# Kernel tuning notes

Hardware: AMD Instinct MI355X
Metric: run time of the kernel (lower is better)

Reference implementation:

```python
import jax, jax.numpy as jnp
import numpy as np

N_MEL = 80; ARNN = 1024; ADIM = 128; EMB = 512; PRE = 256; DRNN = 1024; NF = 32; KS = 31
B = 32; NCTX = 512; T = 500
PAD = (KS - 1) // 2


def setup_inputs() -> dict:
    key = jax.random.key(0)
    ks = jax.random.split(key, 20)
    g = lambda k, shape: jax.random.normal(k, shape, dtype=jnp.float32) * 0.02
    return {
        "memory": jax.random.normal(ks[0], (B, NCTX, EMB), dtype=jnp.float32),
        "decoder_inputs": jax.random.normal(ks[1], (B, N_MEL, T), dtype=jnp.float32),
        "mask": jnp.zeros((B, NCTX), dtype=bool),
        "prenet_w1": g(ks[2], (PRE, N_MEL)),
        "prenet_w2": g(ks[3], (PRE, PRE)),
        "arnn_wih": g(ks[4], (4 * ARNN, PRE + EMB)),
        "arnn_whh": g(ks[5], (4 * ARNN, ARNN)),
        "arnn_bih": jnp.zeros((4 * ARNN,), jnp.float32),
        "arnn_bhh": jnp.zeros((4 * ARNN,), jnp.float32),
        "q_w": g(ks[6], (ADIM, ARNN)),
        "m_w": g(ks[7], (ADIM, EMB)),
        "loc_conv_w": g(ks[8], (NF, 2, KS)),
        "loc_w": g(ks[9], (ADIM, NF)),
        "v_w": g(ks[10], (ADIM,)),
        "drnn_wih": g(ks[11], (4 * DRNN, ARNN + EMB)),
        "drnn_whh": g(ks[12], (4 * DRNN, DRNN)),
        "drnn_bih": jnp.zeros((4 * DRNN,), jnp.float32),
        "drnn_bhh": jnp.zeros((4 * DRNN,), jnp.float32),
        "proj_w": g(ks[13], (N_MEL, DRNN + EMB)),
        "proj_b": jnp.zeros((N_MEL,), jnp.float32),
        "gate_w": g(ks[14], (1, DRNN + EMB)),
        "gate_b": jnp.zeros((1,), jnp.float32),
    }


def _lstm_cell(x, h, c, wih, whh, bih, bhh):
    # PyTorch LSTMCell gate order: i, f, g, o
    z = x @ wih.T + h @ whh.T + bih + bhh
    i, f, g, o = jnp.split(z, 4, axis=-1)
    c2 = jax.nn.sigmoid(f) * c + jax.nn.sigmoid(i) * jnp.tanh(g)
    h2 = jax.nn.sigmoid(o) * jnp.tanh(c2)
    return h2, c2


def reference(memory, decoder_inputs, mask,
              prenet_w1, prenet_w2,
              arnn_wih, arnn_whh, arnn_bih, arnn_bhh,
              q_w, m_w, loc_conv_w, loc_w, v_w,
              drnn_wih, drnn_whh, drnn_bih, drnn_bhh,
              proj_w, proj_b, gate_w, gate_b):
    b, n_ctx, emb = memory.shape
    n_mel, t_out = decoder_inputs.shape[1], decoder_inputs.shape[2]

    # (time, batch, n_mel) with a leading zero go-frame; PreNet (eval: no dropout)
    x = jnp.transpose(decoder_inputs, (2, 0, 1))
    x = jnp.concatenate([jnp.zeros((1, b, n_mel), x.dtype), x], axis=0)
    h = jax.nn.relu(x @ prenet_w1.T)
    h = jax.nn.relu(h @ prenet_w2.T)  # (T+1, B, PRE)
    inputs = h[:-1]  # T decoder steps

    proc_mem = memory @ m_w.T  # (B, n_ctx, ADIM)

    def step(carry, xin):
        ah, ac, dh, dc, aw, awc, actx = carry
        cell_in = jnp.concatenate([xin, actx], axis=-1)
        ah, ac = _lstm_cell(cell_in, ah, ac, arnn_wih, arnn_whh, arnn_bih, arnn_bhh)
        # location-sensitive attention
        aw_cat = jnp.stack([aw, awc], axis=1)  # (B, 2, n_ctx)
        loc = jax.lax.conv_general_dilated(
            aw_cat, loc_conv_w, window_strides=(1,), padding=[(PAD, PAD)],
            dimension_numbers=("NCH", "OIH", "NCH"))  # (B, NF, n_ctx)
        loc = jnp.transpose(loc, (0, 2, 1)) @ loc_w.T  # (B, n_ctx, ADIM)
        q = (ah @ q_w.T)[:, None, :]  # (B, 1, ADIM)
        e = jnp.tanh(q + proc_mem + loc) @ v_w  # (B, n_ctx)
        e = jnp.where(mask, -1e9, e)
        aw = jax.nn.softmax(e, axis=-1)
        actx = jnp.einsum("bn,bne->be", aw, memory)
        awc = awc + aw
        din = jnp.concatenate([ah, actx], axis=-1)
        dh, dc = _lstm_cell(din, dh, dc, drnn_wih, drnn_whh, drnn_bih, drnn_bhh)
        dhc = jnp.concatenate([dh, actx], axis=-1)
        mel = dhc @ proj_w.T + proj_b  # (B, n_mel)
        gate = dhc @ gate_w.T + gate_b  # (B, 1)
        return (ah, ac, dh, dc, aw, awc, actx), (mel, gate[:, 0])

    z32 = lambda *s: jnp.zeros(s, memory.dtype)
    carry0 = (z32(b, ARNN), z32(b, ARNN), z32(b, DRNN), z32(b, DRNN),
              z32(b, n_ctx), z32(b, n_ctx), z32(b, emb))
    _, (mels, gates) = jax.lax.scan(step, carry0, inputs)
    mel_out = jnp.transpose(mels, (1, 2, 0))   # (B, n_mel, T)
    gate_out = jnp.transpose(gates, (1, 0))    # (B, T)
    return mel_out, gate_out
```

## Files before the change

### kernel.cpp

```cpp
#include <hip/hip_runtime.h>

#define NBLK 256
#define NTHR 1024

constexpr int kNMel = 80, kArnn = 1024, kAdim = 128, kEmb = 512, kPre = 256;
constexpr int kNF = 32, kKS = 31, kB = 32, kNctx = 512, kT = 500, kPad = 15;

constexpr int KT_A = 56;
constexpr int KT_D = 80;
constexpr int KT_ALL = KT_A + KT_D;

constexpr int OFF_PREB   = 0;
constexpr int OFF_PROCMB = OFF_PREB + kT * kB * kPre / 2;
constexpr int OFF_QWTB   = OFF_PROCMB + kB * kNctx * kAdim / 2;
constexpr int OFF_LWT    = OFF_QWTB + kAdim * kArnn / 2;
constexpr int OFF_STATE  = OFF_LWT + kAdim * 33;
constexpr int OFF_AHB    = OFF_STATE;
constexpr int OFF_DHB    = OFF_AHB + 2 * kB * kArnn / 2;
constexpr int OFF_DH     = OFF_DHB + 2 * kB * kArnn / 2;
constexpr int OFF_AC     = OFF_DH + 2 * kB * kArnn;
constexpr int OFF_DC     = OFF_AC + kB * kArnn;
constexpr int OFF_ACTX   = OFF_DC + kB * kArnn;
constexpr int OFF_AW     = OFF_ACTX + kB * kEmb;
constexpr int OFF_AWC    = OFF_AW + kB * kNctx;
constexpr int OFF_PAW    = OFF_AWC + kB * kNctx;
constexpr int OFF_NUM    = OFF_PAW + kB * kNctx;
constexpr int OFF_DEN    = OFF_NUM + 2 * kB * kEmb;
constexpr int OFF_END    = OFF_DEN + 2 * kB;
constexpr int STATE_SZ   = OFF_END - OFF_STATE;
constexpr int OFF_BAR    = OFF_END;
constexpr int BAR_LINES  = 266;
constexpr int OFF_PAN    = OFF_BAR + BAR_LINES * 32;
constexpr int PAN_SZ     = NBLK * KT_ALL * 256;
constexpr int OFF_GMB    = OFF_PAN + PAN_SZ;
constexpr int GMB_SZ     = kB * kNctx * kEmb / 2;

typedef __attribute__((ext_vector_type(4))) float fvec4;
typedef __attribute__((ext_vector_type(8))) short bh8_t;
typedef unsigned long long u64;
typedef unsigned short ushortt;

union U64u { u64 u; float2 f2; ushortt s[4]; };

union SMem {
  struct { ushortt xs[16][2048]; } x1;
  struct { float zra[8][2][64][4]; float zrd[8][2][64][4];
           float hb[2][32][4]; } x2;
  struct { float ahb_s[kArnn]; float vw_s[kAdim]; float psum[1024]; float q_s[kAdim];
           float aw_s[96]; float awc_s[96]; float cw[kNF * 2 * kKS];
           float loc_s[64 * 33]; float p_s[64]; float lwt[kAdim * 33];
           float dhc[kArnn + kEmb]; float pprj[126];
           ushortt pm[64 * kAdim]; } b;
  struct { float x8[8][80]; float h1[8][256]; } p;
  struct { float mem_s[4][512]; } m;
};

__device__ __forceinline__ float sigf(float x) { return 1.0f / (1.0f + __expf(-x)); }
__device__ __forceinline__ float tanhfast(float x) { return 1.0f - 2.0f / (__expf(2.0f * x) + 1.0f); }

__device__ __forceinline__ ushortt bf16rn(float f) {
  unsigned u = __float_as_uint(f);
  unsigned r = (u + 0x7FFFu + ((u >> 16) & 1u)) >> 16;
  return (ushortt)r;
}
__device__ __forceinline__ float bf2f(ushortt v) {
  return __uint_as_float((unsigned)v << 16);
}

__device__ __forceinline__ u64 ald64(const void* p) {
  return __hip_atomic_load((const u64*)p, __ATOMIC_RELAXED, __HIP_MEMORY_SCOPE_AGENT);
}
__device__ __forceinline__ float alf(const float* p) {
  return __hip_atomic_load(p, __ATOMIC_RELAXED, __HIP_MEMORY_SCOPE_AGENT);
}
__device__ __forceinline__ void asf(float* p, float v) {
  __hip_atomic_store(p, v, __ATOMIC_RELAXED, __HIP_MEMORY_SCOPE_AGENT);
}
__device__ __forceinline__ void as64(void* p, u64 v) {
  __hip_atomic_store((u64*)p, v, __ATOMIC_RELAXED, __HIP_MEMORY_SCOPE_AGENT);
}
__device__ __forceinline__ unsigned alu(const unsigned* p) {
  return __hip_atomic_load(p, __ATOMIC_RELAXED, __HIP_MEMORY_SCOPE_AGENT);
}
__device__ __forceinline__ void asu(unsigned* p, unsigned v) {
  __hip_atomic_store(p, v, __ATOMIC_RELAXED, __HIP_MEMORY_SCOPE_AGENT);
}

__device__ __forceinline__ void gbar_full(unsigned* cnt, unsigned* gen, unsigned& genv) {
  __syncthreads();
  if (threadIdx.x == 0) {
    __threadfence();
    unsigned arrived = __hip_atomic_fetch_add(cnt, 1u, __ATOMIC_ACQ_REL, __HIP_MEMORY_SCOPE_AGENT) + 1u;
    if (arrived == (unsigned)NBLK) {
      __hip_atomic_store(cnt, 0u, __ATOMIC_RELAXED, __HIP_MEMORY_SCOPE_AGENT);
      __hip_atomic_fetch_add(gen, 1u, __ATOMIC_ACQ_REL, __HIP_MEMORY_SCOPE_AGENT);
    } else {
      while (__hip_atomic_load(gen, __ATOMIC_ACQUIRE, __HIP_MEMORY_SCOPE_AGENT) == genv) {
        __builtin_amdgcn_s_sleep(2);
      }
    }
    ++genv;
  }
  __syncthreads();
}

__device__ __forceinline__ void gbar_light(unsigned* bar, unsigned target, int bk, int tid) {
  asm volatile("s_waitcnt vmcnt(0) lgkmcnt(0)" ::: "memory");
  __syncthreads();
  if (bk == 0) {
    if (tid < 64) {
      if (tid == 0) asm volatile("s_waitcnt vmcnt(0)" ::: "memory");
      unsigned i0 = (unsigned)tid * 4, i1 = i0 + 1, i2 = i0 + 2, i3 = i0 + 3;
      for (;;) {
        bool ok = true;
        if (i0 != 0) ok = ok && (alu(&bar[i0 * 32]) >= target);
        ok = ok && (alu(&bar[i1 * 32]) >= target);
        ok = ok && (alu(&bar[i2 * 32]) >= target);
        ok = ok && (alu(&bar[i3 * 32]) >= target);
        if (__all(ok)) break;
        __builtin_amdgcn_s_sleep(1);
      }
      if (tid < 8) asu(&bar[(256 + tid) * 32], target);
    }
  } else {
    if (tid == 0) {
      asm volatile("s_waitcnt vmcnt(0)" ::: "memory");
      asu(&bar[bk * 32], target);
      unsigned* wk = &bar[(256 + (bk & 7)) * 32];
      while (alu(wk) < target) __builtin_amdgcn_s_sleep(1);
    }
  }
  __syncthreads();
}

template<int LS, int W>
__device__ __forceinline__ void lstm_wave(
    const ushortt* __restrict__ s0, const ushortt* __restrict__ s2,
    const float* __restrict__ numq, const float* __restrict__ invden,
    const short* __restrict__ pan,
    int l, ushortt* xs, fvec4& z0, fvec4& z1)
{
  constexpr int NC  = LS ? 5 : (W < 4 ? 4 : 3);
  constexpr int CB  = LS ? W * 320 : (W < 4 ? W * 256 : 1024 + (W - 4) * 192);
  constexpr int KT0 = CB / 32;
  constexpr int BD0 = LS ? 1024 : 256;
  constexpr int BD1 = LS ? 1536 : 768;
  const int u8 = l & 15, rj = l >> 4;
  const int m = l & 15, kg = l >> 4;

  #pragma unroll
  for (int c = 0; c < NC; ++c) {
    const int c0 = CB + c * 64;
    u64 L[8];
    if (c0 >= BD0 && c0 < BD1) {
      const float* base = numq + (c0 - BD0) + u8 * 4;
      #pragma unroll
      for (int j = 0; j < 8; ++j) {
        int row = 4 * j + rj;
        const float* fp = base + (size_t)row * kEmb;
        U64u a, b2; a.u = ald64(fp); b2.u = ald64(fp + 2);
        float s = invden[row];
        U64u pk;
        pk.s[0] = bf16rn(a.f2.x * s);  pk.s[1] = bf16rn(a.f2.y * s);
        pk.s[2] = bf16rn(b2.f2.x * s); pk.s[3] = bf16rn(b2.f2.y * s);
        L[j] = pk.u;
      }
    } else {
      const ushortt* bsrc; int stride; bool coh;
      if (c0 < BD0) { bsrc = s0 + c0;       stride = (LS ? 1024 : 256); coh = (LS == 1); }
      else          { bsrc = s2 + c0 - BD1; stride = 1024;              coh = true; }
      #pragma unroll
      for (int j = 0; j < 8; ++j) {
        const ushortt* ap = bsrc + (size_t)(4 * j + rj) * stride + u8 * 4;
        L[j] = coh ? ald64(ap) : *reinterpret_cast<const u64*>(ap);
      }
    }
    bh8_t f0 = *reinterpret_cast<const bh8_t*>(pan + (size_t)(KT0 + c * 2) * 512 + l * 8);
    bh8_t f1 = *reinterpret_cast<const bh8_t*>(pan + (size_t)(KT0 + c * 2 + 1) * 512 + l * 8);
    #pragma unroll
    for (int j = 0; j < 8; ++j) {
      int row = 4 * j + rj;
      int sw = u8 ^ ((row & 7) << 1);
      *reinterpret_cast<u64*>(xs + row * 64 + sw * 4) = L[j];
    }
    #pragma unroll
    for (int kt = 0; kt < 2; ++kt) {
      int sw = (2 * (kt * 4 + kg)) ^ ((m & 7) << 1);
      bh8_t a0 = *reinterpret_cast<const bh8_t*>(xs + m * 64 + sw * 4);
      bh8_t a1 = *reinterpret_cast<const bh8_t*>(xs + (16 + m) * 64 + sw * 4);
      bh8_t f = kt ? f1 : f0;
      z0 = __builtin_amdgcn_mfma_f32_16x16x32_bf16(a0, f, z0, 0, 0, 0);
      z1 = __builtin_amdgcn_mfma_f32_16x16x32_bf16(a1, f, z1, 0, 0, 0);
    }
  }
}

extern "C" __global__ void __launch_bounds__(NTHR, 4)
decoder_kernel(const float* __restrict__ gmem, const float* __restrict__ dec,
               const unsigned char* __restrict__ mask,
               const float* __restrict__ pw1, const float* __restrict__ pw2,
               const float* __restrict__ awih, const float* __restrict__ awhh,
               const float* __restrict__ abih, const float* __restrict__ abhh,
               const float* __restrict__ qw, const float* __restrict__ mw,
               const float* __restrict__ cvw, const float* __restrict__ locw,
               const float* __restrict__ vw,
               const float* __restrict__ dwih, const float* __restrict__ dwhh,
               const float* __restrict__ dbih, const float* __restrict__ dbhh,
               const float* __restrict__ pjw, const float* __restrict__ pjb,
               const float* __restrict__ gw, const float* __restrict__ gb,
               float* __restrict__ out, float* __restrict__ ws, int useg)
{
  __shared__ SMem sm;
  __shared__ float s_invden[32];
  const int bk = blockIdx.x, tid = threadIdx.x;
  unsigned genv_f = 0, bcnt = 0;
  unsigned* bar = reinterpret_cast<unsigned*>(ws + OFF_BAR);
  unsigned* cntF = &bar[264 * 32];
  unsigned* genF = &bar[265 * 32];

  ushortt* PREBu = reinterpret_cast<ushortt*>(ws + OFF_PREB);
  ushortt* PROCMBu = reinterpret_cast<ushortt*>(ws + OFF_PROCMB);
  ushortt* QWTBu = reinterpret_cast<ushortt*>(ws + OFF_QWTB);
  float* LWT = ws + OFF_LWT;
  ushortt* AHBu = reinterpret_cast<ushortt*>(ws + OFF_AHB);
  ushortt* DHBu = reinterpret_cast<ushortt*>(ws + OFF_DHB);
  float* DH = ws + OFF_DH;
  float* AC = ws + OFF_AC;
  float* DC = ws + OFF_DC;
  float* ACTX = ws + OFF_ACTX;
  float* AWp = ws + OFF_AW;
  float* AWC = ws + OFF_AWC;
  float* PAW = ws + OFF_PAW;
  float* NUM = ws + OFF_NUM;
  float* DEN = ws + OFF_DEN;
  short* PANS = reinterpret_cast<short*>(ws + OFF_PAN);
  ushortt* GMB = reinterpret_cast<ushortt*>(ws + OFF_GMB);

  for (int i = bk * NTHR + tid; i < STATE_SZ; i += NBLK * NTHR) (ws + OFF_STATE)[i] = 0.f;
  for (int i = bk * NTHR + tid; i < kAdim * kArnn; i += NBLK * NTHR)
    QWTBu[i] = bf16rn(qw[i]);
  for (int i = bk * NTHR + tid; i < kAdim * kNF; i += NBLK * NTHR) {
    int d = i >> 5, f = i & 31;
    LWT[d * 33 + f] = locw[i];
  }
  gbar_full(cntF, genF, genv_f);

  if (bk == 0 && tid < 2 * kB) asf(&DEN[tid], 1.0f);
  for (int it = 0; it < 16; ++it) {
    int task0 = bk * 64 + it * 4;
    for (int i = tid; i < 2048; i += NTHR) {
      int pr = i >> 9, h = i & 511;
      sm.m.mem_s[pr][h] = gmem[(size_t)(task0 + pr) * kEmb + h];
    }
    __syncthreads();
    if (tid < 512) {
      int pr = tid >> 7, d = tid & 127;
      const float* mwr = mw + d * kEmb;
      float acc = 0.f;
      for (int h = 0; h < kEmb; ++h) acc = fmaf(sm.m.mem_s[pr][h], mwr[h], acc);
      PROCMBu[(size_t)(task0 + pr) * kAdim + d] = bf16rn(acc);
    }
    if (useg) {
      for (int i = tid; i < 2048; i += NTHR) {
        int pr = i >> 9, h = i & 511;
        GMB[(size_t)(task0 + pr) * kEmb + h] = bf16rn(sm.m.mem_s[pr][h]);
      }
    }
    __syncthreads();
  }
  for (int g = bk; g < 2000; g += NBLK) {
    int t_idx = g >> 2;
    int b0 = (g & 3) * 8;
    if (t_idx == 0) {
      for (int i = tid; i < 8 * kPre; i += NTHR)
        PREBu[(size_t)(b0 + (i >> 8)) * kPre + (i & 255)] = 0;
      continue;
    }
    for (int i = tid; i < 640; i += NTHR) {
      int bb = i / 80, m2 = i % 80;
      sm.p.x8[bb][m2] = dec[((size_t)(b0 + bb) * kNMel + m2) * kT + (t_idx - 1)];
    }
    __syncthreads();
    if (tid < 512) {
      int u = tid & 255, rep = tid >> 8;
      float acc[4] = {0.f, 0.f, 0.f, 0.f};
      for (int m2 = 0; m2 < 80; ++m2) {
        float w = pw1[u * kNMel + m2];
        #pragma unroll
        for (int r = 0; r < 4; ++r) acc[r] = fmaf(w, sm.p.x8[rep * 4 + r][m2], acc[r]);
      }
      #pragma unroll
      for (int r = 0; r < 4; ++r) sm.p.h1[rep * 4 + r][u] = fmaxf(acc[r], 0.f);
    }
    __syncthreads();
    if (tid < 512) {
      int u = tid & 255, rep = tid >> 8;
      float acc[4] = {0.f, 0.f, 0.f, 0.f};
      for (int k = 0; k < kPre; ++k) {
        float w = pw2[u * kPre + k];
        #pragma unroll
        for (int r = 0; r < 4; ++r) acc[r] = fmaf(w, sm.p.h1[rep * 4 + r][k], acc[r]);
      }
      #pragma unroll
      for (int r = 0; r < 4; ++r)
        PREBu[((size_t)t_idx * kB + b0 + rep * 4 + r) * kPre + u] = bf16rn(fmaxf(acc[r], 0.f));
    }
    __syncthreads();
  }
  {
    const int UNITS = NBLK * KT_ALL * 64;
    for (int u = bk * NTHR + tid; u < UNITS; u += NBLK * NTHR) {
      int bkk = u / (KT_ALL * 64);
      int rem = u - bkk * (KT_ALL * 64);
      int kta = rem >> 6, l = rem & 63;
      int lstm = (kta >= KT_A);
      int kt = lstm ? kta - KT_A : kta;
      int n = l & 15, kg = l >> 4;
      int r = (n >> 2) * 1024 + bkk * 4 + (n & 3);
      bh8_t v;
      #pragma unroll
      for (int j = 0; j < 8; ++j) {
        int k = kt * 32 + kg * 8 + j;
        float wv;
        if (!lstm) wv = (k < 768) ? awih[(size_t)r * 768 + k] : awhh[(size_t)r * 1024 + (k - 768)];
        else       wv = (k < 1536) ? dwih[(size_t)r * 1536 + k] : dwhh[(size_t)r * 1024 + (k - 1536)];
        v[j] = (short)bf16rn(wv);
      }
      *reinterpret_cast<bh8_t*>(PANS + (size_t)u * 8) = v;
    }
  }
  gbar_full(cntF, genF, genv_f);

  for (int t = 0; t <= kT; ++t) {
    const int p = t & 1, q = p ^ 1;
    float* nump = NUM + p * kB * kEmb;
    const float* numq = NUM + q * kB * kEmb;

    if (tid < kB) s_invden[tid] = 1.0f / alf(DEN + q * kB + tid);
    __syncthreads();
    if (t > 0 && tid < 64) {
      int idx = bk * 64 + tid;
      int b2 = idx >> 9;
      float invd = s_invden[b2];
      float av = PAW[idx] * invd;
      asf(&AWp[idx], av);
      asf(&AWC[idx], alf(&AWC[idx]) + av);
      asf(&ACTX[idx], alf(&numq[idx]) * invd);
    }
    if (t < kT) {
      if (tid < 64) asf(&nump[bk * 64 + tid], 0.f);
      if (bk == 0 && tid < kB) asf(DEN + p * kB + tid, 0.f);
    }
    {
      const int wid = tid >> 6, l = tid & 63;
      fvec4 z0 = {0.f, 0.f, 0.f, 0.f}, z1 = z0;
      const ushortt* AHBq_ = AHBu + q * kB * kArnn;
      const ushortt* DHBp_ = DHBu + p * kB * kArnn;
      const ushortt* preb_t = PREBu + (size_t)t * kB * kPre;
      ushortt* xs = &sm.x1.xs[wid][0];
      const short* panb = PANS + (size_t)bk * (KT_ALL * 512);
      const short* pand = panb + KT_A * 512;
      if (wid < 8) {
        if (t < kT) {
          switch (wid) {
            case 0: lstm_wave<0,0>(preb_t, AHBq_, numq, s_invden, panb, l, xs, z0, z1); break;
            case 1: lstm_wave<0,1>(preb_t, AHBq_, numq, s_invden, panb, l, xs, z0, z1); break;
            case 2: lstm_wave<0,2>(preb_t, AHBq_, numq, s_invden, panb, l, xs, z0, z1); break;
            case 3: lstm_wave<0,3>(preb_t, AHBq_, numq, s_invden, panb, l, xs, z0, z1); break;
            case 4: lstm_wave<0,4>(preb_t, AHBq_, numq, s_invden, panb, l, xs, z0, z1); break;
            case 5: lstm_wave<0,5>(preb_t, AHBq_, numq, s_invden, panb, l, xs, z0, z1); break;
            case 6: lstm_wave<0,6>(preb_t, AHBq_, numq, s_invden, panb, l, xs, z0, z1); break;
            default: lstm_wave<0,7>(preb_t, AHBq_, numq, s_invden, panb, l, xs, z0, z1); break;
          }
        }
      } else {
        if (t > 0) {
          switch (wid) {
            case 8:  lstm_wave<1,0>(AHBq_, DHBp_, numq, s_invden, pand, l, xs, z0, z1); break;
            case 9:  lstm_wave<1,1>(AHBq_, DHBp_, numq, s_invden, pand, l, xs, z0, z1); break;
            case 10: lstm_wave<1,2>(AHBq_, DHBp_, numq, s_invden, pand, l, xs, z0, z1); break;
            case 11: lstm_wave<1,3>(AHBq_, DHBp_, numq, s_invden, pand, l, xs, z0, z1); break;
            case 12: lstm_wave<1,4>(AHBq_, DHBp_, numq, s_invden, pand, l, xs, z0, z1); break;
            case 13: lstm_wave<1,5>(AHBq_, DHBp_, numq, s_invden, pand, l, xs, z0, z1); break;
            case 14: lstm_wave<1,6>(AHBq_, DHBp_, numq, s_invden, pand, l, xs, z0, z1); break;
            default: lstm_wave<1,7>(AHBq_, DHBp_, numq, s_invden, pand, l, xs, z0, z1); break;
          }
        }
      }
      __syncthreads();
      if (wid < 8) {
        *reinterpret_cast<fvec4*>(&sm.x2.zra[wid][0][l][0]) = z0;
        *reinterpret_cast<fvec4*>(&sm.x2.zra[wid][1][l][0]) = z1;
      } else {
        *reinterpret_cast<fvec4*>(&sm.x2.zrd[wid - 8][0][l][0]) = z0;
        *reinterpret_cast<fvec4*>(&sm.x2.zrd[wid - 8][1][l][0]) = z1;
      }
    }
    __syncthreads();
    if (tid < 256) {
      const int ls = tid >> 7, uu = (tid >> 5) & 3, b = tid & 31;
      const bool go = (ls == 0) ? (t < kT) : (t > 0);
      if (go) {
        const int mt = b >> 4, mm = b & 15;
        const int lane_base = (mm >> 2) * 16, rr = mm & 3;
        float zg[4];
        #pragma unroll
        for (int g = 0; g < 4; ++g) {
          int ln = lane_base + g * 4 + uu;
          float s = 0.f;
          if (ls == 0) {
            #pragma unroll
            for (int w = 0; w < 8; ++w) s += sm.x2.zra[w][mt][ln][rr];
          } else {
            #pragma unroll
            for (int w = 0; w < 8; ++w) s += sm.x2.zrd[w][mt][ln][rr];
          }
          int rg = g * 1024 + bk * 4 + uu;
          s += (ls ? dbih[rg] + dbhh[rg] : abih[rg] + abhh[rg]);
          zg[g] = s;
        }
        float* cst = ls ? DC : AC;
        const int idx = b * kArnn + bk * 4 + uu;
        float c = sigf(zg[1]) * cst[idx] + sigf(zg[0]) * tanhfast(zg[2]);
        cst[idx] = c;
        float h = sigf(zg[3]) * tanhfast(c);
        if (ls) asf(&DH[q * kB * kArnn + idx], h);
        sm.x2.hb[ls][b][uu] = h;
      }
    }
    __syncthreads();
    if (tid < 64) {
      int ls = tid >> 5, b = tid & 31;
      bool go2 = ls ? (t > 0) : (t < kT);
      if (go2) {
        U64u pk;
        #pragma unroll
        for (int j = 0; j < 4; ++j) pk.s[j] = bf16rn(sm.x2.hb[ls][b][j]);
        ushortt* dst = (ls ? (DHBu + q * kB * kArnn) : (AHBu + p * kB * kArnn)) + b * kArnn + bk * 4;
        as64(dst, pk.u);
      }
    }
    gbar_light(bar, ++bcnt, bk, tid);

    if (t < kT) {
      const int b = bk >> 3, sub = bk & 7, j0 = sub * 64;
      const int pbase = (sub == 0) ? 0 : 21 + (sub - 1) * 20;
      const int pcnt = (sub == 0) ? 21 : 20;
      const ushortt* AHBp_ = AHBu + p * kB * kArnn;
      if (tid < 256) {
        U64u v; v.u = ald64(AHBp_ + b * kArnn + tid * 4);
        #pragma unroll
        for (int j = 0; j < 4; ++j) sm.b.ahb_s[tid * 4 + j] = bf2f(v.s[j]);
      }
      for (int i = tid; i < 94; i += NTHR) {
        int jj = j0 - kPad + i;
        bool ok = (jj >= 0 && jj < kNctx);
        sm.b.aw_s[i] = ok ? alf(&AWp[b * kNctx + jj]) : 0.f;
        sm.b.awc_s[i] = ok ? alf(&AWC[b * kNctx + jj]) : 0.f;
      }
      for (int i = tid; i < kNF * 2 * kKS; i += NTHR) sm.b.cw[i] = cvw[i];
      for (int i = tid; i < kAdim * 33; i += NTHR) sm.b.lwt[i] = LWT[i];
      for (int i = tid; i < kAdim; i += NTHR) sm.b.vw_s[i] = vw[i];
      {
        const fvec4* src = reinterpret_cast<const fvec4*>(PROCMBu + (size_t)(b * kNctx + j0) * kAdim);
        fvec4* dst = reinterpret_cast<fvec4*>(sm.b.pm);
        for (int i = tid; i < 1024; i += NTHR) dst[i] = src[i];
      }
      if (sub < 4 && t > 0) {
        for (int i = tid; i < kArnn + kEmb; i += NTHR)
          sm.b.dhc[i] = (i < kArnn) ? alf(&DH[q * kB * kArnn + b * kArnn + i])
                                    : alf(&ACTX[b * kEmb + (i - kArnn)]);
      }
      __syncthreads();
      {
        int d = tid & 127, qr = tid >> 7;
        const ushortt* wq = QWTBu + (size_t)d * kArnn + qr * 128;
        const float* ahs = sm.b.ahb_s + qr * 128;
        float acc = 0.f;
        #pragma unroll 4
        for (int h8 = 0; h8 < 16; ++h8) {
          U64u a, c2;
          a.u = *reinterpret_cast<const u64*>(wq + h8 * 8);
          c2.u = *reinterpret_cast<const u64*>(wq + h8 * 8 + 4);
          #pragma unroll
          for (int j = 0; j < 4; ++j) acc = fmaf(bf2f(a.s[j]), ahs[h8 * 8 + j], acc);
          #pragma unroll
          for (int j = 0; j < 4; ++j) acc = fmaf(bf2f(c2.s[j]), ahs[h8 * 8 + 4 + j], acc);
        }
        sm.b.psum[tid] = acc;
      }
      __syncthreads();
      if (tid < kAdim) {
        float s = 0.f;
        #pragma unroll
        for (int k = 0; k < 8; ++k) s += sm.b.psum[tid + 128 * k];
        sm.b.q_s[tid] = s;
      }
      if (tid < 512) {
        int j = tid >> 3, f0 = (tid & 7) * 4;
        #pragma unroll
        for (int fi = 0; fi < 4; ++fi) {
          int f = f0 + fi;
          const float* w0 = &sm.b.cw[f * 62];
          float s = 0.f;
          for (int k = 0; k < kKS; ++k)
            s = fmaf(sm.b.aw_s[j + k], w0[k], fmaf(sm.b.awc_s[j + k], w0[31 + k], s));
          sm.b.loc_s[j * 33 + f] = s;
        }
      }
      if (sub < 4 && t > 0 && tid < pcnt * 6) {
        int ol = tid / 6, kc = tid % 6, og = pbase + ol;
        const float* row = (og < kNMel) ? pjw + (size_t)og * (kArnn + kEmb) : gw;
        const float* x = sm.b.dhc + kc * 256;
        const float* r2 = row + kc * 256;
        float acc = 0.f;
        for (int k = 0; k < 256; ++k) acc = fmaf(r2[k], x[k], acc);
        sm.b.pprj[tid] = acc;
      }
      __syncthreads();
      if (tid < 512) {
        int j = tid >> 3, grp = tid & 7, jj = j0 + j;
        float pe = 0.f;
        #pragma unroll 4
        for (int dd = 0; dd < 16; ++dd) {
          int d = grp + 8 * dd;
          float l2 = 0.f;
          const float* ls2 = &sm.b.loc_s[j * 33];
          const float* lw2 = &sm.b.lwt[d * 33];
          #pragma unroll 8
          for (int f = 0; f < kNF; ++f) l2 = fmaf(ls2[f], lw2[f], l2);
          float x = sm.b.q_s[d] + bf2f(sm.b.pm[j * kAdim + d]) + l2;
          pe = fmaf(sm.b.vw_s[d], tanhfast(x), pe);
        }
        pe += __shfl_xor(pe, 1);
        pe += __shfl_xor(pe, 2);
        pe += __shfl_xor(pe, 4);
        if (grp == 0) {
          float pv = mask[b * kNctx + jj] ? 0.f : __expf(pe);
          sm.b.p_s[j] = pv;
          PAW[b * kNctx + jj] = pv;
        }
      }
      if (sub < 4 && t > 0 && tid < pcnt) {
        int og = pbase + tid;
        float val = (og < kNMel) ? pjb[og] : gb[0];
        #pragma unroll
        for (int kc = 0; kc < 6; ++kc) val += sm.b.pprj[tid * 6 + kc];
        if (og < kNMel) out[((size_t)b * kNMel + og) * kT + (t - 1)] = val;
        else out[(size_t)kB * kNMel * kT + b * kT + (t - 1)] = val;
      }
      __syncthreads();
      if (tid < 64) {
        float v = sm.b.p_s[tid];
        #pragma unroll
        for (int o = 1; o < 64; o <<= 1) v += __shfl_xor(v, o);
        if (tid == 0) atomicAdd(DEN + p * kB + b, v);
      }
      {
        int col = tid & 511, half = tid >> 9;
        int jbase = half * 32;
        if (useg) {
          const ushortt* memb = GMB + (size_t)(b * kNctx + j0 + jbase) * kEmb + col;
          float a0 = 0.f, a1 = 0.f, a2 = 0.f, a3 = 0.f;
          #pragma unroll 4
          for (int jj2 = 0; jj2 < 32; jj2 += 4) {
            a0 = fmaf(sm.b.p_s[jbase + jj2],     bf2f(memb[(size_t)jj2 * kEmb]), a0);
            a1 = fmaf(sm.b.p_s[jbase + jj2 + 1], bf2f(memb[(size_t)(jj2 + 1) * kEmb]), a1);
            a2 = fmaf(sm.b.p_s[jbase + jj2 + 2], bf2f(memb[(size_t)(jj2 + 2) * kEmb]), a2);
            a3 = fmaf(sm.b.p_s[jbase + jj2 + 3], bf2f(memb[(size_t)(jj2 + 3) * kEmb]), a3);
          }
          atomicAdd(&nump[b * kEmb + col], (a0 + a1) + (a2 + a3));
        } else {
          const float* memb = gmem + (size_t)(b * kNctx + j0 + jbase) * kEmb + col;
          float a0 = 0.f, a1 = 0.f;
          #pragma unroll 8
          for (int jj2 = 0; jj2 < 32; jj2 += 2) {
            a0 = fmaf(sm.b.p_s[jbase + jj2], memb[(size_t)jj2 * kEmb], a0);
            a1 = fmaf(sm.b.p_s[jbase + jj2 + 1], memb[(size_t)(jj2 + 1) * kEmb], a1);
          }
          atomicAdd(&nump[b * kEmb + col], a0 + a1);
        }
      }
      gbar_light(bar, ++bcnt, bk, tid);
    }
  }

  if (bk < kB) {
    const int b = bk;
    for (int i = tid; i < kArnn + kEmb; i += NTHR)
      sm.b.dhc[i] = (i < kArnn) ? alf(&DH[1 * kB * kArnn + b * kArnn + i])
                                : alf(&ACTX[b * kEmb + (i - kArnn)]);
    __syncthreads();
    if (tid < 486) {
      int ol = tid / 6, kc = tid % 6;
      const float* row = (ol < kNMel) ? pjw + (size_t)ol * (kArnn + kEmb) : gw;
      const float* x = sm.b.dhc + kc * 256;
      const float* r2 = row + kc * 256;
      float acc = 0.f;
      for (int k = 0; k < 256; ++k) acc = fmaf(r2[k], x[k], acc);
      sm.b.psum[tid] = acc;
    }
    __syncthreads();
    if (tid < 81) {
      float val = (tid < kNMel) ? pjb[tid] : gb[0];
      #pragma unroll
      for (int kc = 0; kc < 6; ++kc) val += sm.b.psum[tid * 6 + kc];
      if (tid < kNMel) out[((size_t)b * kNMel + tid) * kT + (kT - 1)] = val;
      else out[(size_t)kB * kNMel * kT + b * kT + (kT - 1)] = val;
    }
  }
}

extern "C" void kernel_launch(void* const* d_in, const int* in_sizes, int n_in,
                              void* d_out, int out_size, void* d_ws, size_t ws_size,
                              hipStream_t stream) {
  const float* gmem = (const float*)d_in[0];
  const float* dec = (const float*)d_in[1];
  const unsigned char* mask = (const unsigned char*)d_in[2];
  const float* pw1 = (const float*)d_in[3];
  const float* pw2 = (const float*)d_in[4];
  const float* awih = (const float*)d_in[5];
  const float* awhh = (const float*)d_in[6];
  const float* abih = (const float*)d_in[7];
  const float* abhh = (const float*)d_in[8];
  const float* qw = (const float*)d_in[9];
  const float* mw = (const float*)d_in[10];
  const float* cvw = (const float*)d_in[11];
  const float* locw = (const float*)d_in[12];
  const float* vw = (const float*)d_in[13];
  const float* dwih = (const float*)d_in[14];
  const float* dwhh = (const float*)d_in[15];
  const float* dbih = (const float*)d_in[16];
  const float* dbhh = (const float*)d_in[17];
  const float* pjw = (const float*)d_in[18];
  const float* pjb = (const float*)d_in[19];
  const float* gw = (const float*)d_in[20];
  const float* gb = (const float*)d_in[21];
  float* out = (float*)d_out;
  float* ws = (float*)d_ws;

  int useg = (ws_size >= (size_t)(OFF_GMB + GMB_SZ) * sizeof(float)) ? 1 : 0;

  hipMemsetAsync((char*)d_ws + (size_t)OFF_BAR * sizeof(float), 0,
                 (size_t)BAR_LINES * 128, stream);
  hipLaunchKernelGGL(decoder_kernel, dim3(NBLK), dim3(NTHR), 0, stream,
                     gmem, dec, mask, pw1, pw2, awih, awhh, abih, abhh, qw, mw,
                     cvw, locw, vw, dwih, dwhh, dbih, dbhh, pjw, pjb, gw, gb,
                     out, ws, useg);
}
```

Baseline: 43.28 ms.

## Keep each block's memory slice and processed-memory tile resident in LDS

Each persistent block now keeps its fixed 64-row slice of the encoder memory (as bf16) and of the processed memory in a dedicated LDS region, loaded once before the time loop. The per-step context-vector accumulation and attention-energy computation read from LDS instead of global or L2 memory. The two half-block partial sums are also combined in LDS before a single atomic add per column, halving the atomics. The trade-off is a large increase in static shared memory, about 80 KB more, which may reduce occupancy or exceed LDS limits alongside the existing unions. It also removes the fp32 fallback path that was used when the workspace was too small.

```diff
diff --git a/kernel.cpp b/kernel.cpp
--- a/kernel.cpp
+++ b/kernel.cpp
@@ -32,8 +32,6 @@
 constexpr int BAR_LINES  = 266;
 constexpr int OFF_PAN    = OFF_BAR + BAR_LINES * 32;
 constexpr int PAN_SZ     = NBLK * KT_ALL * 256;
-constexpr int OFF_GMB    = OFF_PAN + PAN_SZ;
-constexpr int GMB_SZ     = kB * kNctx * kEmb / 2;
 
 typedef __attribute__((ext_vector_type(4))) float fvec4;
 typedef __attribute__((ext_vector_type(8))) short bh8_t;
@@ -42,17 +40,20 @@
 
 union U64u { u64 u; float2 f2; ushortt s[4]; };
 
-union SMem {
-  struct { ushortt xs[16][2048]; } x1;
-  struct { float zra[8][2][64][4]; float zrd[8][2][64][4];
-           float hb[2][32][4]; } x2;
-  struct { float ahb_s[kArnn]; float vw_s[kAdim]; float psum[1024]; float q_s[kAdim];
-           float aw_s[96]; float awc_s[96]; float cw[kNF * 2 * kKS];
-           float loc_s[64 * 33]; float p_s[64]; float lwt[kAdim * 33];
-           float dhc[kArnn + kEmb]; float pprj[126];
-           ushortt pm[64 * kAdim]; } b;
-  struct { float x8[8][80]; float h1[8][256]; } p;
-  struct { float mem_s[4][512]; } m;
+struct SMemS {
+  ushortt gmb[64 * kEmb];
+  ushortt pm[64 * kAdim];
+  union {
+    struct { ushortt xs[16][2048]; } x1;
+    struct { float zra[8][2][64][4]; float zrd[8][2][64][4];
+             float hb[2][32][4]; } x2;
+    struct { float ahb_s[kArnn]; float vw_s[kAdim]; float psum[1024]; float q_s[kAdim];
+             float aw_s[96]; float awc_s[96]; float cw[kNF * 2 * kKS];
+             float loc_s[64 * 33]; float p_s[64]; float lwt[kAdim * 33];
+             float dhc[kArnn + kEmb]; float pprj[126]; } b;
+    struct { float x8[8][80]; float h1[8][256]; } p;
+    struct { float mem_s[4][512]; } m;
+  } u;
 };
 
 __device__ __forceinline__ float sigf(float x) { return 1.0f / (1.0f + __expf(-x)); }
@@ -208,9 +209,9 @@
                const float* __restrict__ dbih, const float* __restrict__ dbhh,
                const float* __restrict__ pjw, const float* __restrict__ pjb,
                const float* __restrict__ gw, const float* __restrict__ gb,
-               float* __restrict__ out, float* __restrict__ ws, int useg)
+               float* __restrict__ out, float* __restrict__ ws)
 {
-  __shared__ SMem sm;
+  __shared__ SMemS sm;
   __shared__ float s_invden[32];
   const int bk = blockIdx.x, tid = threadIdx.x;
   unsigned genv_f = 0, bcnt = 0;
@@ -234,7 +235,6 @@
   float* NUM = ws + OFF_NUM;
   float* DEN = ws + OFF_DEN;
   short* PANS = reinterpret_cast<short*>(ws + OFF_PAN);
-  ushortt* GMB = reinterpret_cast<ushortt*>(ws + OFF_GMB);
 
   for (int i = bk * NTHR + tid; i < STATE_SZ; i += NBLK * NTHR) (ws + OFF_STATE)[i] = 0.f;
   for (int i = bk * NTHR + tid; i < kAdim * kArnn; i += NBLK * NTHR)
@@ -250,24 +250,25 @@
     int task0 = bk * 64 + it * 4;
     for (int i = tid; i < 2048; i += NTHR) {
       int pr = i >> 9, h = i & 511;
-      sm.m.mem_s[pr][h] = gmem[(size_t)(task0 + pr) * kEmb + h];
+      sm.u.m.mem_s[pr][h] = gmem[(size_t)(task0 + pr) * kEmb + h];
     }
     __syncthreads();
     if (tid < 512) {
       int pr = tid >> 7, d = tid & 127;
       const float* mwr = mw + d * kEmb;
       float acc = 0.f;
-      for (int h = 0; h < kEmb; ++h) acc = fmaf(sm.m.mem_s[pr][h], mwr[h], acc);
+      for (int h = 0; h < kEmb; ++h) acc = fmaf(sm.u.m.mem_s[pr][h], mwr[h], acc);
       PROCMBu[(size_t)(task0 + pr) * kAdim + d] = bf16rn(acc);
     }
-    if (useg) {
-      for (int i = tid; i < 2048; i += NTHR) {
-        int pr = i >> 9, h = i & 511;
-        GMB[(size_t)(task0 + pr) * kEmb + h] = bf16rn(sm.m.mem_s[pr][h]);
-      }
-    }
-    __syncthreads();
-  }
+    __syncthreads();
+  }
+  for (int i = tid; i < 64 * kEmb; i += NTHR) {
+    int j = i >> 9, h = i & 511;
+    sm.gmb[i] = bf16rn(gmem[((size_t)bk * 64 + j) * kEmb + h]);
+  }
+  for (int i = tid; i < 64 * kAdim; i += NTHR)
+    sm.pm[i] = PROCMBu[(size_t)bk * 64 * kAdim + i];
+  __syncthreads();
   for (int g = bk; g < 2000; g += NBLK) {
     int t_idx = g >> 2;
     int b0 = (g & 3) * 8;
@@ -278,7 +279,7 @@
     }
     for (int i = tid; i < 640; i += NTHR) {
       int bb = i / 80, m2 = i % 80;
-      sm.p.x8[bb][m2] = dec[((size_t)(b0 + bb) * kNMel + m2) * kT + (t_idx - 1)];
+      sm.u.p.x8[bb][m2] = dec[((size_t)(b0 + bb) * kNMel + m2) * kT + (t_idx - 1)];
     }
     __syncthreads();
     if (tid < 512) {
@@ -287,10 +288,10 @@
       for (int m2 = 0; m2 < 80; ++m2) {
         float w = pw1[u * kNMel + m2];
         #pragma unroll
-        for (int r = 0; r < 4; ++r) acc[r] = fmaf(w, sm.p.x8[rep * 4 + r][m2], acc[r]);
+        for (int r = 0; r < 4; ++r) acc[r] = fmaf(w, sm.u.p.x8[rep * 4 + r][m2], acc[r]);
       }
       #pragma unroll
-      for (int r = 0; r < 4; ++r) sm.p.h1[rep * 4 + r][u] = fmaxf(acc[r], 0.f);
+      for (int r = 0; r < 4; ++r) sm.u.p.h1[rep * 4 + r][u] = fmaxf(acc[r], 0.f);
     }
     __syncthreads();
     if (tid < 512) {
@@ -299,7 +300,7 @@
       for (int k = 0; k < kPre; ++k) {
         float w = pw2[u * kPre + k];
         #pragma unroll
-        for (int r = 0; r < 4; ++r) acc[r] = fmaf(w, sm.p.h1[rep * 4 + r][k], acc[r]);
+        for (int r = 0; r < 4; ++r) acc[r] = fmaf(w, sm.u.p.h1[rep * 4 + r][k], acc[r]);
       }
       #pragma unroll
       for (int r = 0; r < 4; ++r)
@@ -357,7 +358,7 @@
       const ushortt* AHBq_ = AHBu + q * kB * kArnn;
       const ushortt* DHBp_ = DHBu + p * kB * kArnn;
       const ushortt* preb_t = PREBu + (size_t)t * kB * kPre;
-      ushortt* xs = &sm.x1.xs[wid][0];
+      ushortt* xs = &sm.u.x1.xs[wid][0];
       const short* panb = PANS + (size_t)bk * (KT_ALL * 512);
       const short* pand = panb + KT_A * 512;
       if (wid < 8) {
@@ -389,11 +390,11 @@
       }
       __syncthreads();
       if (wid < 8) {
-        *reinterpret_cast<fvec4*>(&sm.x2.zra[wid][0][l][0]) = z0;
-        *reinterpret_cast<fvec4*>(&sm.x2.zra[wid][1][l][0]) = z1;
+        *reinterpret_cast<fvec4*>(&sm.u.x2.zra[wid][0][l][0]) = z0;
+        *reinterpret_cast<fvec4*>(&sm.u.x2.zra[wid][1][l][0]) = z1;
       } else {
-        *reinterpret_cast<fvec4*>(&sm.x2.zrd[wid - 8][0][l][0]) = z0;
-        *reinterpret_cast<fvec4*>(&sm.x2.zrd[wid - 8][1][l][0]) = z1;
+        *reinterpret_cast<fvec4*>(&sm.u.x2.zrd[wid - 8][0][l][0]) = z0;
+        *reinterpret_cast<fvec4*>(&sm.u.x2.zrd[wid - 8][1][l][0]) = z1;
       }
     }
     __syncthreads();
@@ -410,10 +411,10 @@
           float s = 0.f;
           if (ls == 0) {
             #pragma unroll
-            for (int w = 0; w < 8; ++w) s += sm.x2.zra[w][mt][ln][rr];
+            for (int w = 0; w < 8; ++w) s += sm.u.x2.zra[w][mt][ln][rr];
           } else {
             #pragma unroll
-            for (int w = 0; w < 8; ++w) s += sm.x2.zrd[w][mt][ln][rr];
+            for (int w = 0; w < 8; ++w) s += sm.u.x2.zrd[w][mt][ln][rr];
           }
           int rg = g * 1024 + bk * 4 + uu;
           s += (ls ? dbih[rg] + dbhh[rg] : abih[rg] + abhh[rg]);
@@ -425,7 +426,7 @@
         cst[idx] = c;
         float h = sigf(zg[3]) * tanhfast(c);
         if (ls) asf(&DH[q * kB * kArnn + idx], h);
-        sm.x2.hb[ls][b][uu] = h;
+        sm.u.x2.hb[ls][b][uu] = h;
       }
     }
     __syncthreads();
@@ -435,7 +436,7 @@
       if (go2) {
         U64u pk;
         #pragma unroll
-        for (int j = 0; j < 4; ++j) pk.s[j] = bf16rn(sm.x2.hb[ls][b][j]);
+        for (int j = 0; j < 4; ++j) pk.s[j] = bf16rn(sm.u.x2.hb[ls][b][j]);
         ushortt* dst = (ls ? (DHBu + q * kB * kArnn) : (AHBu + p * kB * kArnn)) + b * kArnn + bk * 4;
         as64(dst, pk.u);
       }
@@ -450,32 +451,27 @@
       if (tid < 256) {
         U64u v; v.u = ald64(AHBp_ + b * kArnn + tid * 4);
         #pragma unroll
-        for (int j = 0; j < 4; ++j) sm.b.ahb_s[tid * 4 + j] = bf2f(v.s[j]);
+        for (int j = 0; j < 4; ++j) sm.u.b.ahb_s[tid * 4 + j] = bf2f(v.s[j]);
       }
       for (int i = tid; i < 94; i += NTHR) {
         int jj = j0 - kPad + i;
         bool ok = (jj >= 0 && jj < kNctx);
-        sm.b.aw_s[i] = ok ? alf(&AWp[b * kNctx + jj]) : 0.f;
-        sm.b.awc_s[i] = ok ? alf(&AWC[b * kNctx + jj]) : 0.f;
-      }
-      for (int i = tid; i < kNF * 2 * kKS; i += NTHR) sm.b.cw[i] = cvw[i];
-      for (int i = tid; i < kAdim * 33; i += NTHR) sm.b.lwt[i] = LWT[i];
-      for (int i = tid; i < kAdim; i += NTHR) sm.b.vw_s[i] = vw[i];
-      {
-        const fvec4* src = reinterpret_cast<const fvec4*>(PROCMBu + (size_t)(b * kNctx + j0) * kAdim);
-        fvec4* dst = reinterpret_cast<fvec4*>(sm.b.pm);
-        for (int i = tid; i < 1024; i += NTHR) dst[i] = src[i];
-      }
+        sm.u.b.aw_s[i] = ok ? alf(&AWp[b * kNctx + jj]) : 0.f;
+        sm.u.b.awc_s[i] = ok ? alf(&AWC[b * kNctx + jj]) : 0.f;
+      }
+      for (int i = tid; i < kNF * 2 * kKS; i += NTHR) sm.u.b.cw[i] = cvw[i];
+      for (int i = tid; i < kAdim * 33; i += NTHR) sm.u.b.lwt[i] = LWT[i];
+      for (int i = tid; i < kAdim; i += NTHR) sm.u.b.vw_s[i] = vw[i];
       if (sub < 4 && t > 0) {
         for (int i = tid; i < kArnn + kEmb; i += NTHR)
-          sm.b.dhc[i] = (i < kArnn) ? alf(&DH[q * kB * kArnn + b * kArnn + i])
-                                    : alf(&ACTX[b * kEmb + (i - kArnn)]);
+          sm.u.b.dhc[i] = (i < kArnn) ? alf(&DH[q * kB * kArnn + b * kArnn + i])
+                                      : alf(&ACTX[b * kEmb + (i - kArnn)]);
       }
       __syncthreads();
       {
         int d = tid & 127, qr = tid >> 7;
         const ushortt* wq = QWTBu + (size_t)d * kArnn + qr * 128;
-        const float* ahs = sm.b.ahb_s + qr * 128;
+        const float* ahs = sm.u.b.ahb_s + qr * 128;
         float acc = 0.f;
         #pragma unroll 4
         for (int h8 = 0; h8 < 16; ++h8) {
@@ -487,35 +483,35 @@
           #pragma unroll
           for (int j = 0; j < 4; ++j) acc = fmaf(bf2f(c2.s[j]), ahs[h8 * 8 + 4 + j], acc);
         }
-        sm.b.psum[tid] = acc;
+        sm.u.b.psum[tid] = acc;
       }
       __syncthreads();
       if (tid < kAdim) {
         float s = 0.f;
         #pragma unroll
-        for (int k = 0; k < 8; ++k) s += sm.b.psum[tid + 128 * k];
-        sm.b.q_s[tid] = s;
+        for (int k = 0; k < 8; ++k) s += sm.u.b.psum[tid + 128 * k];
+        sm.u.b.q_s[tid] = s;
       }
       if (tid < 512) {
         int j = tid >> 3, f0 = (tid & 7) * 4;
         #pragma unroll
         for (int fi = 0; fi < 4; ++fi) {
           int f = f0 + fi;
-          const float* w0 = &sm.b.cw[f * 62];
+          const float* w0 = &sm.u.b.cw[f * 62];
           float s = 0.f;
           for (int k = 0; k < kKS; ++k)
-            s = fmaf(sm.b.aw_s[j + k], w0[k], fmaf(sm.b.awc_s[j + k], w0[31 + k], s));
-          sm.b.loc_s[j * 33 + f] = s;
+            s = fmaf(sm.u.b.aw_s[j + k], w0[k], fmaf(sm.u.b.awc_s[j + k], w0[31 + k], s));
+          sm.u.b.loc_s[j * 33 + f] = s;
         }
       }
       if (sub < 4 && t > 0 && tid < pcnt * 6) {
         int ol = tid / 6, kc = tid % 6, og = pbase + ol;
         const float* row = (og < kNMel) ? pjw + (size_t)og * (kArnn + kEmb) : gw;
-        const float* x = sm.b.dhc + kc * 256;
+        const float* x = sm.u.b.dhc + kc * 256;
         const float* r2 = row + kc * 256;
         float acc = 0.f;
         for (int k = 0; k < 256; ++k) acc = fmaf(r2[k], x[k], acc);
-        sm.b.pprj[tid] = acc;
+        sm.u.b.pprj[tid] = acc;
       }
       __syncthreads();
       if (tid < 512) {
@@ -525,19 +521,19 @@
         for (int dd = 0; dd < 16; ++dd) {
           int d = grp + 8 * dd;
           float l2 = 0.f;
-          const float* ls2 = &sm.b.loc_s[j * 33];
-          const float* lw2 = &sm.b.lwt[d * 33];
+          const float* ls2 = &sm.u.b.loc_s[j * 33];
+          const float* lw2 = &sm.u.b.lwt[d * 33];
           #pragma unroll 8
           for (int f = 0; f < kNF; ++f) l2 = fmaf(ls2[f], lw2[f], l2);
-          float x = sm.b.q_s[d] + bf2f(sm.b.pm[j * kAdim + d]) + l2;
-          pe = fmaf(sm.b.vw_s[d], tanhfast(x), pe);
+          float x = sm.u.b.q_s[d] + bf2f(sm.pm[j * kAdim + d]) + l2;
+          pe = fmaf(sm.u.b.vw_s[d], tanhfast(x), pe);
         }
         pe += __shfl_xor(pe, 1);
         pe += __shfl_xor(pe, 2);
         pe += __shfl_xor(pe, 4);
         if (grp == 0) {
           float pv = mask[b * kNctx + jj] ? 0.f : __expf(pe);
-          sm.b.p_s[j] = pv;
+          sm.u.b.p_s[j] = pv;
           PAW[b * kNctx + jj] = pv;
         }
       }
@@ -545,42 +541,34 @@
         int og = pbase + tid;
         float val = (og < kNMel) ? pjb[og] : gb[0];
         #pragma unroll
-        for (int kc = 0; kc < 6; ++kc) val += sm.b.pprj[tid * 6 + kc];
+        for (int kc = 0; kc < 6; ++kc) val += sm.u.b.pprj[tid * 6 + kc];
         if (og < kNMel) out[((size_t)b * kNMel + og) * kT + (t - 1)] = val;
         else out[(size_t)kB * kNMel * kT + b * kT + (t - 1)] = val;
       }
       __syncthreads();
       if (tid < 64) {
-        float v = sm.b.p_s[tid];
+        float v = sm.u.b.p_s[tid];
         #pragma unroll
         for (int o = 1; o < 64; o <<= 1) v += __shfl_xor(v, o);
         if (tid == 0) atomicAdd(DEN + p * kB + b, v);
       }
+      float nsum;
       {
         int col = tid & 511, half = tid >> 9;
-        int jbase = half * 32;
-        if (useg) {
-          const ushortt* memb = GMB + (size_t)(b * kNctx + j0 + jbase) * kEmb + col;
-          float a0 = 0.f, a1 = 0.f, a2 = 0.f, a3 = 0.f;
-          #pragma unroll 4
-          for (int jj2 = 0; jj2 < 32; jj2 += 4) {
-            a0 = fmaf(sm.b.p_s[jbase + jj2],     bf2f(memb[(size_t)jj2 * kEmb]), a0);
-            a1 = fmaf(sm.b.p_s[jbase + jj2 + 1], bf2f(memb[(size_t)(jj2 + 1) * kEmb]), a1);
-            a2 = fmaf(sm.b.p_s[jbase + jj2 + 2], bf2f(memb[(size_t)(jj2 + 2) * kEmb]), a2);
-            a3 = fmaf(sm.b.p_s[jbase + jj2 + 3], bf2f(memb[(size_t)(jj2 + 3) * kEmb]), a3);
-          }
-          atomicAdd(&nump[b * kEmb + col], (a0 + a1) + (a2 + a3));
-        } else {
-          const float* memb = gmem + (size_t)(b * kNctx + j0 + jbase) * kEmb + col;
-          float a0 = 0.f, a1 = 0.f;
-          #pragma unroll 8
-          for (int jj2 = 0; jj2 < 32; jj2 += 2) {
-            a0 = fmaf(sm.b.p_s[jbase + jj2], memb[(size_t)jj2 * kEmb], a0);
-            a1 = fmaf(sm.b.p_s[jbase + jj2 + 1], memb[(size_t)(jj2 + 1) * kEmb], a1);
-          }
-          atomicAdd(&nump[b * kEmb + col], a0 + a1);
-        }
-      }
+        const ushortt* memb = sm.gmb + (size_t)(half * 32) * kEmb + col;
+        float a0 = 0.f, a1 = 0.f, a2 = 0.f, a3 = 0.f;
+        #pragma unroll 4
+        for (int jj2 = 0; jj2 < 32; jj2 += 4) {
+          a0 = fmaf(sm.u.b.p_s[half * 32 + jj2],     bf2f(memb[(size_t)jj2 * kEmb]), a0);
+          a1 = fmaf(sm.u.b.p_s[half * 32 + jj2 + 1], bf2f(memb[(size_t)(jj2 + 1) * kEmb]), a1);
+          a2 = fmaf(sm.u.b.p_s[half * 32 + jj2 + 2], bf2f(memb[(size_t)(jj2 + 2) * kEmb]), a2);
+          a3 = fmaf(sm.u.b.p_s[half * 32 + jj2 + 3], bf2f(memb[(size_t)(jj2 + 3) * kEmb]), a3);
+        }
+        nsum = (a0 + a1) + (a2 + a3);
+        if (half) sm.u.b.psum[col] = nsum;
+      }
+      __syncthreads();
+      if (tid < 512) atomicAdd(&nump[b * kEmb + tid], nsum + sm.u.b.psum[tid]);
       gbar_light(bar, ++bcnt, bk, tid);
     }
   }
@@ -588,23 +576,23 @@
   if (bk < kB) {
     const int b = bk;
     for (int i = tid; i < kArnn + kEmb; i += NTHR)
-      sm.b.dhc[i] = (i < kArnn) ? alf(&DH[1 * kB * kArnn + b * kArnn + i])
-                                : alf(&ACTX[b * kEmb + (i - kArnn)]);
+      sm.u.b.dhc[i] = (i < kArnn) ? alf(&DH[1 * kB * kArnn + b * kArnn + i])
+                                  : alf(&ACTX[b * kEmb + (i - kArnn)]);
     __syncthreads();
     if (tid < 486) {
       int ol = tid / 6, kc = tid % 6;
       const float* row = (ol < kNMel) ? pjw + (size_t)ol * (kArnn + kEmb) : gw;
-      const float* x = sm.b.dhc + kc * 256;
+      const float* x = sm.u.b.dhc + kc * 256;
       const float* r2 = row + kc * 256;
       float acc = 0.f;
       for (int k = 0; k < 256; ++k) acc = fmaf(r2[k], x[k], acc);
-      sm.b.psum[tid] = acc;
+      sm.u.b.psum[tid] = acc;
     }
     __syncthreads();
     if (tid < 81) {
       float val = (tid < kNMel) ? pjb[tid] : gb[0];
       #pragma unroll
-      for (int kc = 0; kc < 6; ++kc) val += sm.b.psum[tid * 6 + kc];
+      for (int kc = 0; kc < 6; ++kc) val += sm.u.b.psum[tid * 6 + kc];
       if (tid < kNMel) out[((size_t)b * kNMel + tid) * kT + (kT - 1)] = val;
       else out[(size_t)kB * kNMel * kT + b * kT + (kT - 1)] = val;
     }
@@ -639,12 +627,10 @@
   float* out = (float*)d_out;
   float* ws = (float*)d_ws;
 
-  int useg = (ws_size >= (size_t)(OFF_GMB + GMB_SZ) * sizeof(float)) ? 1 : 0;
-
   hipMemsetAsync((char*)d_ws + (size_t)OFF_BAR * sizeof(float), 0,
                  (size_t)BAR_LINES * 128, stream);
   hipLaunchKernelGGL(decoder_kernel, dim3(NBLK), dim3(NTHR), 0, stream,
                      gmem, dec, mask, pw1, pw2, awih, awhh, abih, abhh, qw, mw,
                      cvw, locw, vw, dwih, dwhh, dbih, dbhh, pjw, pjb, gw, gb,
-                     out, ws, useg);
-}
+                     out, ws);
+}
```

After: 42.56 ms. Within noise of the previous version (-1.6%).
